# Optimization experiments

Hardware: AMD Instinct MI355X
Metric: run time of the kernel (lower is better)

## Reference

```python
import jax, jax.numpy as jnp
import numpy as np

QLEN, MLEN, CMLEN, BSZ, D_MODEL = 1024, 1024, 512, 2, 1024
N_HEAD, D_HEAD, D_INNER = 16, 64, 4096
KLEN = MLEN + CMLEN + QLEN
LN_EPS = 1e-5


def _layer_norm(x, scale, bias):
    mu = jnp.mean(x, axis=-1, keepdims=True)
    var = jnp.var(x, axis=-1, keepdims=True)
    return (x - mu) * jax.lax.rsqrt(var + LN_EPS) * scale + bias


def _rel_shift(x):
    # x: [qlen, klen, bsz, n_head]  (Transformer-XL relative shift)
    q, k, b, n = x.shape
    x = jnp.concatenate([jnp.zeros((q, 1, b, n), x.dtype), x], axis=1)
    x = x.reshape(k + 1, q, b, n)[1:]
    return x.reshape(q, k, b, n)


def setup_inputs() -> dict:
    key = jax.random.key(0)
    ks = jax.random.split(key, 10)
    s = 0.02
    # causal mask: query i (absolute pos MLEN_TOT+i) cannot attend to key j > MLEN_TOT+i
    mlen_tot = KLEN - QLEN
    i = jnp.arange(QLEN)[:, None]
    j = jnp.arange(KLEN)[None, :]
    attn_mask = j > (i + mlen_tot)
    return {
        "input_ids": jax.random.normal(ks[0], (QLEN, BSZ, D_MODEL), jnp.float32),
        "pos_emb": jax.random.normal(ks[1], (KLEN, D_MODEL), jnp.float32),
        "mem": jax.random.normal(ks[2], (MLEN, BSZ, D_MODEL), jnp.float32),
        "c_mem": jax.random.normal(ks[3], (CMLEN, BSZ, D_MODEL), jnp.float32),
        "attn_mask": attn_mask,
        "qkv_w": jax.random.normal(ks[4], (D_MODEL, 3 * N_HEAD * D_HEAD), jnp.float32) * s,
        "r_w": jax.random.normal(ks[5], (D_MODEL, N_HEAD * D_HEAD), jnp.float32) * s,
        "o_w": jax.random.normal(ks[6], (N_HEAD * D_HEAD, D_MODEL), jnp.float32) * s,
        "r_w_bias": jax.random.normal(ks[7], (N_HEAD, D_HEAD), jnp.float32) * s,
        "r_r_bias": jax.random.normal(ks[8], (N_HEAD, D_HEAD), jnp.float32) * s,
        "ln_attn_scale": jnp.ones((D_MODEL,), jnp.float32),
        "ln_attn_bias": jnp.zeros((D_MODEL,), jnp.float32),
        "ff_w1": jax.random.normal(ks[9], (D_MODEL, D_INNER), jnp.float32) * s,
        "ff_b1": jnp.zeros((D_INNER,), jnp.float32),
        "ff_w2": jax.random.normal(jax.random.fold_in(key, 11), (D_INNER, D_MODEL), jnp.float32) * s,
        "ff_b2": jnp.zeros((D_MODEL,), jnp.float32),
        "ln_ff_scale": jnp.ones((D_MODEL,), jnp.float32),
        "ln_ff_bias": jnp.zeros((D_MODEL,), jnp.float32),
    }


def reference(input_ids, pos_emb, mem, c_mem, attn_mask, qkv_w, r_w, o_w,
              r_w_bias, r_r_bias, ln_attn_scale, ln_attn_bias,
              ff_w1, ff_b1, ff_w2, ff_b2, ln_ff_scale, ln_ff_bias):
    qlen, bsz, d_model = input_ids.shape
    n_head, d_head = r_w_bias.shape
    scale = 1.0 / np.sqrt(d_head)

    # _concat_memories + cat with current sequence (seq-first, dim 0)
    mems = jnp.concatenate([mem, c_mem], axis=0)
    cat = jnp.concatenate([mems, input_ids], axis=0)          # [klen, b, d]

    w_heads = cat @ qkv_w                                     # [klen, b, 3*h*dh]
    w_q, w_k, w_v = jnp.split(w_heads, 3, axis=-1)
    w_q = w_q[-qlen:]
    klen = w_k.shape[0]

    w_q = w_q.reshape(qlen, bsz, n_head, d_head)
    w_k = w_k.reshape(klen, bsz, n_head, d_head)
    w_v = w_v.reshape(klen, bsz, n_head, d_head)
    r_k = (pos_emb @ r_w).reshape(klen, n_head, d_head)       # [klen, h, dh]

    AC = jnp.einsum('ibnd,jbnd->ijbn', w_q + r_w_bias, w_k)
    BD = jnp.einsum('ibnd,jnd->ijbn', w_q + r_r_bias, r_k)
    BD = _rel_shift(BD)
    attn_score = (AC + BD) * scale                            # [q, k, b, h]

    attn_score = jnp.where(attn_mask[:, :, None, None], jnp.float32(-1e30), attn_score)
    attn_prob = jax.nn.softmax(attn_score, axis=1)

    attn_vec = jnp.einsum('ijbn,jbnd->ibnd', attn_prob, w_v)
    attn_vec = attn_vec.reshape(qlen, bsz, n_head * d_head)
    attn_out = attn_vec @ o_w

    # post-lnorm residual (pre_lnorm=False)
    attn_res = _layer_norm(input_ids + attn_out, ln_attn_scale, ln_attn_bias)

    # PositionwiseFF (post-lnorm)
    h = jax.nn.relu(attn_res @ ff_w1 + ff_b1) @ ff_w2 + ff_b2
    out = _layer_norm(attn_res + h, ln_ff_scale, ln_ff_bias)
    return out
```

## Files before the change

kernel.cpp:

```cpp
#include <hip/hip_runtime.h>
#include <hip/hip_bf16.h>

#define QLEN 1024
#define KLEN 2560
#define MTOT 1536
#define BSZ 2
#define NH 16
#define DH 64
#define DMODEL 1024
#define DINNER 4096

typedef short bf16x8 __attribute__((ext_vector_type(8)));
typedef float f32x4  __attribute__((ext_vector_type(4)));

__device__ __forceinline__ short f2bf(float f) {
    union { float f; unsigned u; } v; v.f = f;
    unsigned r = v.u + 0x7FFFu + ((v.u >> 16) & 1u);
    return (short)(r >> 16);
}
__device__ __forceinline__ float bf2f(short s) {
    union { unsigned u; float f; } v; v.u = ((unsigned)(unsigned short)s) << 16;
    return v.f;
}
__device__ __forceinline__ unsigned pack2(float a, float b) {
    unsigned pk;
    asm("v_cvt_pk_bf16_f32 %0, %1, %2" : "=v"(pk) : "v"(a), "v"(b));
    return pk;
}

#define GLOAD16(g, l)                                                        \
    __builtin_amdgcn_global_load_lds(                                        \
        (const __attribute__((address_space(1))) unsigned int*)(g),          \
        (__attribute__((address_space(3))) unsigned int*)(l), 16, 0, 0)

__device__ __forceinline__ void tr_body(
    const float* __restrict__ in, short* __restrict__ out,
    int K, int N, int bx, int by, int tid, float (*ts)[65])
{
    const int k0 = by * 64, n0 = bx * 64;
    const int r = tid >> 2, cb = (tid & 3) * 16;
    #pragma unroll
    for (int u = 0; u < 16; u += 4) {
        const float4 v = *(const float4*)(in + (size_t)(k0 + r) * N + n0 + cb + u);
        ts[r][cb + u] = v.x; ts[r][cb + u + 1] = v.y;
        ts[r][cb + u + 2] = v.z; ts[r][cb + u + 3] = v.w;
    }
    __syncthreads();
    #pragma unroll
    for (int p = 0; p < 4; p++) {
        const int wr_ = (tid >> 4) + p * 16;
        const int c   = (tid & 15) * 4;
        uint2 pk;
        pk.x = pack2(ts[c][wr_], ts[c + 1][wr_]);
        pk.y = pack2(ts[c + 2][wr_], ts[c + 3][wr_]);
        *(uint2*)(out + (size_t)(n0 + wr_) * K + k0 + c) = pk;
    }
}

__global__ __launch_bounds__(256) void prep_all(
    const float* __restrict__ mem, const float* __restrict__ cmem,
    const float* __restrict__ inp, short* __restrict__ catb,
    const float* __restrict__ pos, short* __restrict__ posb,
    const float* __restrict__ qkv_w, short* __restrict__ qkv_wt,
    const float* __restrict__ r_w, short* __restrict__ r_wt,
    const float* __restrict__ o_w, short* __restrict__ o_wt,
    const float* __restrict__ ff_w1, short* __restrict__ ff1t,
    const float* __restrict__ ff_w2, short* __restrict__ ff2t)
{
    __shared__ float ts[64][65];
    const int bid = blockIdx.x;
    const int tid = threadIdx.x;
    if (bid < 2560) {
        const int i = bid * 256 + tid;
        const int row = i >> 7, c = (i & 127) * 8;
        const float* src;
        if (row < 2048)      src = mem  + (size_t)row * 1024;
        else if (row < 3072) src = cmem + (size_t)(row - 2048) * 1024;
        else                 src = inp  + (size_t)(row - 3072) * 1024;
        const float4 a = *(const float4*)(src + c);
        const float4 b = *(const float4*)(src + c + 4);
        uint4 o;
        o.x = pack2(a.x, a.y); o.y = pack2(a.z, a.w);
        o.z = pack2(b.x, b.y); o.w = pack2(b.z, b.w);
        *(uint4*)(catb + (size_t)i * 8) = o;
    } else if (bid < 3840) {
        const int i = (bid - 2560) * 256 + tid;
        const float4 a = *(const float4*)(pos + (size_t)i * 8);
        const float4 b = *(const float4*)(pos + (size_t)i * 8 + 4);
        uint4 o;
        o.x = pack2(a.x, a.y); o.y = pack2(a.z, a.w);
        o.z = pack2(b.x, b.y); o.w = pack2(b.z, b.w);
        *(uint4*)(posb + (size_t)i * 8) = o;
    } else if (bid < 4608) {
        const int r = bid - 3840; tr_body(qkv_w, qkv_wt, 1024, 3072, r % 48, r / 48, tid, ts);
    } else if (bid < 4864) {
        const int r = bid - 4608; tr_body(r_w, r_wt, 1024, 1024, r % 16, r / 16, tid, ts);
    } else if (bid < 5120) {
        const int r = bid - 4864; tr_body(o_w, o_wt, 1024, 1024, r % 16, r / 16, tid, ts);
    } else if (bid < 6144) {
        const int r = bid - 5120; tr_body(ff_w1, ff1t, 1024, 4096, r % 64, r / 64, tid, ts);
    } else {
        const int r = bid - 6144; tr_body(ff_w2, ff2t, 4096, 1024, r % 16, r / 16, tid, ts);
    }
}

__global__ __launch_bounds__(256) void vt_conv(
    const short* __restrict__ wh, short* __restrict__ vt)
{
    __shared__ short Ts[64][72];
    const int j0 = blockIdx.x * 64;
    const int bn = blockIdx.y;
    const int b = bn >> 4, n = bn & 15;
    const int tid = threadIdx.x;
    {
        const int key = tid >> 2, c = (tid & 3) * 16;
        const short* p = wh + ((size_t)(j0 + key) * BSZ + b) * 3072 + 2048 + n * 64 + c;
        *(bf16x8*)&Ts[key][c]     = *(const bf16x8*)p;
        *(bf16x8*)&Ts[key][c + 8] = *(const bf16x8*)(p + 8);
    }
    __syncthreads();
    {
        const int d = tid >> 2, kc = (tid & 3) * 16;
        __attribute__((aligned(16))) short tmp[16];
        #pragma unroll
        for (int u = 0; u < 16; u++) tmp[u] = Ts[kc + u][d];
        short* q = vt + ((size_t)(bn * 64) + d) * KLEN + j0 + kc;
        *(uint4*)q       = *(uint4*)tmp;
        *(uint4*)(q + 8) = *((uint4*)tmp + 1);
    }
}

__device__ __forceinline__ void gemm_core(
    const short* __restrict__ A, const short* __restrict__ Bt,
    short* As, short* Bs, int Kfull, int klen, int bm, int bn,
    int tid, f32x4 acc[4][4])
{
    const int w  = tid >> 6;
    const int l  = tid & 63;
    const int lg = l >> 4, lc = l & 15;
    const int wr = w >> 1, wc = w & 1;
    const int srow = 2 * w * 16 + (l >> 2);
    const int scol = (l & 3) * 8;
    const size_t aoff0 = (size_t)(bm + srow) * Kfull + scol;
    const size_t boff0 = (size_t)(bn + srow) * Kfull + scol;
    const size_t rstep = (size_t)16 * Kfull;
    short* lA0 = As + 2 * w * 512;
    short* lA1 = As + (2 * w + 1) * 512;
    short* lB0 = Bs + 2 * w * 512;
    short* lB1 = Bs + (2 * w + 1) * 512;

    for (int k0 = 0; k0 < klen; k0 += 32) {
        GLOAD16(A + aoff0 + k0, lA0);
        GLOAD16(A + aoff0 + rstep + k0, lA1);
        GLOAD16(Bt + boff0 + k0, lB0);
        GLOAD16(Bt + boff0 + rstep + k0, lB1);
        __syncthreads();
        bf16x8 af[4], bfr[4];
        #pragma unroll
        for (int m = 0; m < 4; m++)
            af[m] = *(const bf16x8*)(As + (wr * 64 + m * 16 + lc) * 32 + lg * 8);
        #pragma unroll
        for (int n = 0; n < 4; n++)
            bfr[n] = *(const bf16x8*)(Bs + (wc * 64 + n * 16 + lc) * 32 + lg * 8);
        #pragma unroll
        for (int m = 0; m < 4; m++)
            #pragma unroll
            for (int n = 0; n < 4; n++)
                acc[m][n] = __builtin_amdgcn_mfma_f32_16x16x32_bf16(
                    af[m], bfr[n], acc[m][n], 0, 0, 0);
        __syncthreads();
    }
}

__global__ __launch_bounds__(256) void gemm_g12(
    const short* __restrict__ catb, const short* __restrict__ qkv_wt,
    short* __restrict__ whb,
    const short* __restrict__ posb, const short* __restrict__ r_wt,
    short* __restrict__ rkb)
{
    __shared__ short As[4096], Bs[4096];
    const int tid = threadIdx.x;
    const int id0 = blockIdx.x;
    int id = (id0 & 7) * 116 + (id0 >> 3);
    const short *A, *Bt; short* Cb; int N, bm, bn;
    if (id < 384) {
        A = catb; Bt = qkv_wt; Cb = whb; N = 3072;
        bm = (id >> 4) * 128; bn = (8 + (id & 15)) * 128;
    } else if (id < 768) {
        id -= 384;
        A = catb; Bt = qkv_wt; Cb = whb; N = 3072;
        bm = (24 + id / 24) * 128; bn = (id % 24) * 128;
    } else {
        id -= 768;
        A = posb; Bt = r_wt; Cb = rkb; N = 1024;
        bm = (id / 8) * 128; bn = (id % 8) * 128;
    }

    f32x4 acc[4][4];
    #pragma unroll
    for (int m = 0; m < 4; m++)
        #pragma unroll
        for (int n = 0; n < 4; n++) acc[m][n] = (f32x4){0.f, 0.f, 0.f, 0.f};
    gemm_core(A, Bt, As, Bs, 1024, 1024, bm, bn, tid, acc);

    const int w = tid >> 6, l = tid & 63, lg = l >> 4, lc = l & 15;
    const int wr = w >> 1, wc = w & 1;
    #pragma unroll
    for (int m = 0; m < 4; m++)
        #pragma unroll
        for (int n = 0; n < 4; n++) {
            const int col = bn + wc * 64 + n * 16 + lc;
            #pragma unroll
            for (int r = 0; r < 4; r++) {
                const int row = bm + wr * 64 + m * 16 + lg * 4 + r;
                Cb[(size_t)row * N + col] = f2bf(acc[m][n][r]);
            }
        }
}

__global__ __launch_bounds__(256) void gemm_relu(
    const short* __restrict__ A, const short* __restrict__ Bt,
    const float* __restrict__ bias, short* __restrict__ Cb,
    int N, int K)
{
    __shared__ short As[4096], Bs[4096];
    const int tid = threadIdx.x;
    const int nbx = N >> 7;
    const int lid = blockIdx.x;
    const int nwg8 = gridDim.x >> 3;
    const int swz = (lid & 7) * nwg8 + (lid >> 3);
    const int bn = (swz % nbx) * 128, bm = (swz / nbx) * 128;
    f32x4 acc[4][4];
    #pragma unroll
    for (int m = 0; m < 4; m++)
        #pragma unroll
        for (int n = 0; n < 4; n++) acc[m][n] = (f32x4){0.f, 0.f, 0.f, 0.f};
    gemm_core(A, Bt, As, Bs, K, K, bm, bn, tid, acc);

    const int w = tid >> 6, l = tid & 63, lg = l >> 4, lc = l & 15;
    const int wr = w >> 1, wc = w & 1;
    #pragma unroll
    for (int m = 0; m < 4; m++)
        #pragma unroll
        for (int n = 0; n < 4; n++) {
            const int col = bn + wc * 64 + n * 16 + lc;
            const float bv = bias[col];
            #pragma unroll
            for (int r = 0; r < 4; r++) {
                const int row = bm + wr * 64 + m * 16 + lg * 4 + r;
                Cb[(size_t)row * N + col] = f2bf(fmaxf(acc[m][n][r] + bv, 0.0f));
            }
        }
}

__global__ __launch_bounds__(256) void gemm_split(
    const short* __restrict__ A, const short* __restrict__ Bt,
    float* __restrict__ C0, float* __restrict__ C1,
    int N, int Kfull, int Ksub)
{
    __shared__ short As[4096], Bs[4096];
    const int tid = threadIdx.x;
    const int nbx = N >> 7;
    const int lid = blockIdx.x;
    const int nwg8 = gridDim.x >> 3;
    const int swz = (lid & 7) * nwg8 + (lid >> 3);
    const int bn = (swz % nbx) * 128;
    const int rest = swz / nbx;
    const int bm = (rest & 15) * 128;
    const int z = rest >> 4;
    float* C = z ? C1 : C0;
    f32x4 acc[4][4];
    #pragma unroll
    for (int m = 0; m < 4; m++)
        #pragma unroll
        for (int n = 0; n < 4; n++) acc[m][n] = (f32x4){0.f, 0.f, 0.f, 0.f};
    gemm_core(A + z * Ksub, Bt + z * Ksub, As, Bs, Kfull, Ksub, bm, bn, tid, acc);

    const int w = tid >> 6, l = tid & 63, lg = l >> 4, lc = l & 15;
    const int wr = w >> 1, wc = w & 1;
    #pragma unroll
    for (int m = 0; m < 4; m++)
        #pragma unroll
        for (int n = 0; n < 4; n++) {
            const int col = bn + wc * 64 + n * 16 + lc;
            #pragma unroll
            for (int r = 0; r < 4; r++) {
                const int row = bm + wr * 64 + m * 16 + lg * 4 + r;
                C[(size_t)row * N + col] = acc[m][n][r];
            }
        }
}

__global__ __launch_bounds__(512, 2) void attn_mfma(
    const short* __restrict__ wh,
    const short* __restrict__ vt,
    const short* __restrict__ rk,
    const float* __restrict__ rwb,
    const float* __restrict__ rrb,
    short* __restrict__ po,
    float* __restrict__ ml)
{
    __shared__ __align__(16) short Ks[2][64 * 64];
    __shared__ __align__(16) short Vs[2][64 * 64];
    __shared__ __align__(16) short Rs[256 * 64];
    __shared__ __align__(16) short Ps[8][16 * 64];

    const int bid = blockIdx.x;
    const int ibp = (bid >> 3) & 7;
    const int z   = (bid >> 6) & 1;
    const int bn  = ((bid & 7) << 2) | (bid >> 7);
    const int i0  = ibp * 128;
    const int b   = bn >> 4, n = bn & 15;
    const int tid = threadIdx.x;
    const int w   = tid >> 6;
    const int l   = tid & 63;
    const int lg  = l >> 4;
    const int lc  = l & 15;
    const int i_base = i0 + 16 * w;

    bf16x8 aqw[2], aqr[2];
    {
        const int i = i_base + lc;
        const short* qp = wh + ((size_t)(MTOT + i) * BSZ + b) * 3072 + n * 64;
        #pragma unroll
        for (int kc2 = 0; kc2 < 2; kc2++) {
            const bf16x8 q8 = *(const bf16x8*)(qp + kc2 * 32 + lg * 8);
            const int d0 = kc2 * 32 + lg * 8;
            #pragma unroll
            for (int e = 0; e < 8; e++) {
                const float qv = bf2f(q8[e]);
                aqw[kc2][e] = f2bf(qv + rwb[n * 64 + d0 + e]);
                aqr[kc2][e] = f2bf(qv + rrb[n * 64 + d0 + e]);
            }
        }
    }

    f32x4 o_acc[4];
    #pragma unroll
    for (int nt = 0; nt < 4; nt++) o_acc[nt] = (f32x4){0.f, 0.f, 0.f, 0.f};
    float mrun[4]  = {0.f, 0.f, 0.f, 0.f};
    float lpart[4] = {0.f, 0.f, 0.f, 0.f};

    const int jend   = i0 + 1664;
    const int jhalf  = i0 / 2 + 832;
    const int jstart = z ? jhalf : 0;
    const int jstop  = z ? jend  : jhalf;

    const int kr = tid >> 3, kc = tid & 7;
    const size_t whK = (size_t)b * 3072 + 1024 + n * 64;
    const size_t vtK = (size_t)(bn * 64) * KLEN;
    const int mbase0 = jstart - i0 + 896;

    #pragma unroll
    for (int u = 0; u < 3; u++) {
        const int m = mbase0 + kr + 64 * u;
        bf16x8 rv = (bf16x8){0, 0, 0, 0, 0, 0, 0, 0};
        if (m < KLEN)
            rv = *(const bf16x8*)(rk + (size_t)m * 1024 + n * 64 + kc * 8);
        const int slot = m & 255;
        *(bf16x8*)(Rs + slot * 64 + ((kc ^ (slot & 7)) * 8)) = rv;
    }
    {
        const bf16x8 k0 = *(const bf16x8*)(wh + (size_t)(jstart + kr) * (BSZ * 3072) + whK + kc * 8);
        const bf16x8 v0 = *(const bf16x8*)(vt + vtK + (size_t)kr * KLEN + jstart + kc * 8);
        *(bf16x8*)(Ks[0] + kr * 64 + ((kc ^ (kr & 7)) * 8)) = k0;
        *(bf16x8*)(Vs[0] + kr * 64 + ((kc ^ (kr & 7)) * 8)) = v0;
    }
    bf16x8 pk = (bf16x8){0,0,0,0,0,0,0,0}, pv = pk, pr;
    {
        const int jn = jstart + 64;
        if (jn < jstop) {
            pk = *(const bf16x8*)(wh + (size_t)(jn + kr) * (BSZ * 3072) + whK + kc * 8);
            pv = *(const bf16x8*)(vt + vtK + (size_t)kr * KLEN + jn + kc * 8);
        }
        const int m = mbase0 + 192 + kr;
        pr = (m < KLEN) ? *(const bf16x8*)(rk + (size_t)m * 1024 + n * 64 + kc * 8)
                        : (bf16x8){0, 0, 0, 0, 0, 0, 0, 0};
    }

    int cur = 0;
    for (int j0 = jstart; j0 < jstop; j0 += 64) {
        const int mbase = j0 - i0 + 896;
        __syncthreads();
        *(bf16x8*)(Ks[cur ^ 1] + kr * 64 + ((kc ^ (kr & 7)) * 8)) = pk;
        *(bf16x8*)(Vs[cur ^ 1] + kr * 64 + ((kc ^ (kr & 7)) * 8)) = pv;
        {
            const int mw = mbase + 192 + kr;
            const int slot = mw & 255;
            *(bf16x8*)(Rs + slot * 64 + ((kc ^ (slot & 7)) * 8)) = pr;
        }
        {
            const int jn = j0 + 128;
            if (jn < jstop) {
                pk = *(const bf16x8*)(wh + (size_t)(jn + kr) * (BSZ * 3072) + whK + kc * 8);
                pv = *(const bf16x8*)(vt + vtK + (size_t)kr * KLEN + jn + kc * 8);
            }
            const int m = mbase + 256 + kr;
            pr = (m < KLEN) ? *(const bf16x8*)(rk + (size_t)m * 1024 + n * 64 + kc * 8)
                            : (bf16x8){0, 0, 0, 0, 0, 0, 0, 0};
        }

        __builtin_amdgcn_s_setprio(1);
        f32x4 sfr[4];
        #pragma unroll
        for (int jt = 0; jt < 4; jt++) {
            const int row = 16 * jt + lc;
            const int c0 = (lg ^ (row & 7)) * 8, c1 = ((4 + lg) ^ (row & 7)) * 8;
            const bf16x8 bk0 = *(const bf16x8*)(Ks[cur] + row * 64 + c0);
            const bf16x8 bk1 = *(const bf16x8*)(Ks[cur] + row * 64 + c1);
            f32x4 acc = (f32x4){0.f, 0.f, 0.f, 0.f};
            acc = __builtin_amdgcn_mfma_f32_16x16x32_bf16(aqw[0], bk0, acc, 0, 0, 0);
            acc = __builtin_amdgcn_mfma_f32_16x16x32_bf16(aqw[1], bk1, acc, 0, 0, 0);
            sfr[jt] = acc;
        }
        f32x4 dr[5];
        #pragma unroll
        for (int mt = 0; mt < 5; mt++) {
            const int slot = (mbase + 16 * mt + lc + 112 - 16 * w) & 255;
            const int c0 = (lg ^ (slot & 7)) * 8, c1 = ((4 + lg) ^ (slot & 7)) * 8;
            const bf16x8 br0 = *(const bf16x8*)(Rs + slot * 64 + c0);
            const bf16x8 br1 = *(const bf16x8*)(Rs + slot * 64 + c1);
            f32x4 acc = (f32x4){0.f, 0.f, 0.f, 0.f};
            acc = __builtin_amdgcn_mfma_f32_16x16x32_bf16(aqr[0], br0, acc, 0, 0, 0);
            acc = __builtin_amdgcn_mfma_f32_16x16x32_bf16(aqr[1], br1, acc, 0, 0, 0);
            dr[mt] = acc;
        }
        __builtin_amdgcn_s_setprio(0);

        #pragma unroll
        for (int r = 0; r < 4; r++) {
            const int q   = 4 * lg + r;
            const int o   = lc + 15 - q;
            const int src = (l & 48) | (o & 15);
            float sv[4];
            float mx = -1e30f;
            #pragma unroll
            for (int jt = 0; jt < 4; jt++) {
                const float v0 = __shfl(dr[jt][r], src);
                const float v1 = __shfl(dr[jt + 1][r], src);
                const float bd = (o < 16) ? v0 : v1;
                float s = (sfr[jt][r] + bd) * 0.125f;
                if (z) {
                    const int j = j0 + 16 * jt + lc;
                    if (j > i_base + q + MTOT) s = -1e30f;
                }
                sv[jt] = s;
                mx = fmaxf(mx, s);
            }
            if (__any(mx - mrun[r] > 8.0f)) {
                #pragma unroll
                for (int msk = 1; msk <= 8; msk <<= 1)
                    mx = fmaxf(mx, __shfl_xor(mx, msk));
                const float mnew = fmaxf(mrun[r], mx);
                const float corr = __expf(mrun[r] - mnew);
                mrun[r] = mnew;
                lpart[r] *= corr;
                #pragma unroll
                for (int nt = 0; nt < 4; nt++) o_acc[nt][r] *= corr;
            }
            float p0 = __expf(sv[0] - mrun[r]);
            float p1 = __expf(sv[1] - mrun[r]);
            float p2 = __expf(sv[2] - mrun[r]);
            float p3 = __expf(sv[3] - mrun[r]);
            lpart[r] += (p0 + p1) + (p2 + p3);
            const unsigned pk01 = pack2(p0, p1);
            const unsigned pk23 = pack2(p2, p3);
            short* pw = Ps[w] + q * 64 + (lc & 7);
            const int qs = q & 7;
            pw[(((0 + (lc >> 3)) ^ qs) * 8)] = (short)(pk01 & 0xffffu);
            pw[(((2 + (lc >> 3)) ^ qs) * 8)] = (short)(pk01 >> 16);
            pw[(((4 + (lc >> 3)) ^ qs) * 8)] = (short)(pk23 & 0xffffu);
            pw[(((6 + (lc >> 3)) ^ qs) * 8)] = (short)(pk23 >> 16);
        }

        asm volatile("s_waitcnt lgkmcnt(0)" ::: "memory");
        __builtin_amdgcn_sched_barrier(0);

        __builtin_amdgcn_s_setprio(1);
        const int pc0 = (lg ^ (lc & 7)) * 8, pc1 = ((4 + lg) ^ (lc & 7)) * 8;
        const bf16x8 pa0 = *(const bf16x8*)(Ps[w] + lc * 64 + pc0);
        const bf16x8 pa1 = *(const bf16x8*)(Ps[w] + lc * 64 + pc1);
        #pragma unroll
        for (int nt = 0; nt < 4; nt++) {
            const int row = 16 * nt + lc;
            const int c0 = (lg ^ (row & 7)) * 8, c1 = ((4 + lg) ^ (row & 7)) * 8;
            const bf16x8 bv0 = *(const bf16x8*)(Vs[cur] + row * 64 + c0);
            const bf16x8 bv1 = *(const bf16x8*)(Vs[cur] + row * 64 + c1);
            o_acc[nt] = __builtin_amdgcn_mfma_f32_16x16x32_bf16(pa0, bv0, o_acc[nt], 0, 0, 0);
            o_acc[nt] = __builtin_amdgcn_mfma_f32_16x16x32_bf16(pa1, bv1, o_acc[nt], 0, 0, 0);
        }
        __builtin_amdgcn_s_setprio(0);
        cur ^= 1;
    }

    const size_t blk = (size_t)z * 256 + ibp * 32 + bn;
    #pragma unroll
    for (int r = 0; r < 4; r++) {
        float lr = lpart[r];
        #pragma unroll
        for (int msk = 1; msk <= 8; msk <<= 1)
            lr += __shfl_xor(lr, msk);
        const int q = 16 * w + 4 * lg + r;
        #pragma unroll
        for (int nt = 0; nt < 4; nt++)
            po[(blk * 128 + q) * 64 + 16 * nt + lc] = f2bf(o_acc[nt][r]);
        if (lc == 0) {
            ml[(blk * 128 + q) * 2 + 0] = mrun[r];
            ml[(blk * 128 + q) * 2 + 1] = lr;
        }
    }
}

__global__ __launch_bounds__(256) void attn_merge(
    const short* __restrict__ po, const float* __restrict__ ml,
    short* __restrict__ av)
{
    const int blk = blockIdx.x;
    const int ib2 = blk >> 5, bn = blk & 31;
    const int b = bn >> 4, n = bn & 15;
    const int tid = threadIdx.x;
    const int q64 = tid >> 2, dc = (tid & 3) * 16;
    const int i = ib2 * 64 + q64;
    const size_t r0 = ((size_t)(i >> 7) * 32 + bn) * 128 + (i & 127);
    const size_t r1 = ((size_t)(256 + (i >> 7) * 32 + bn)) * 128 + (i & 127);
    const float m0 = ml[r0 * 2], l0 = ml[r0 * 2 + 1];
    const float m1 = ml[r1 * 2], l1 = ml[r1 * 2 + 1];
    const float M = fmaxf(m0, m1);
    const float c0 = __expf(m0 - M), c1 = __expf(m1 - M);
    const float invL = 1.0f / (l0 * c0 + l1 * c1);
    const bf16x8 a0 = *(const bf16x8*)(po + r0 * 64 + dc);
    const bf16x8 a1 = *(const bf16x8*)(po + r0 * 64 + dc + 8);
    const bf16x8 b0 = *(const bf16x8*)(po + r1 * 64 + dc);
    const bf16x8 b1 = *(const bf16x8*)(po + r1 * 64 + dc + 8);
    __attribute__((aligned(16))) short ov[16];
    #pragma unroll
    for (int e = 0; e < 8; e++) {
        ov[e]     = f2bf((bf2f(a0[e]) * c0 + bf2f(b0[e]) * c1) * invL);
        ov[e + 8] = f2bf((bf2f(a1[e]) * c0 + bf2f(b1[e]) * c1) * invL);
    }
    short* op = av + ((size_t)i * BSZ + b) * 1024 + n * 64 + dc;
    *(uint4*)op       = *(uint4*)ov;
    *(uint4*)(op + 8) = *((uint4*)ov + 1);
}

template <bool WB, bool HASB>
__global__ __launch_bounds__(256) void ln_fuse(
    const float* __restrict__ p0, const float* __restrict__ p1,
    const float* __restrict__ badd, const float* __restrict__ res,
    const float* __restrict__ scale, const float* __restrict__ bias,
    float* __restrict__ out, short* __restrict__ outb)
{
    const int row = blockIdx.x;
    const int tid = threadIdx.x;
    const size_t base = (size_t)row * 1024 + tid * 4;
    const float4 a = *(const float4*)(p0 + base);
    const float4 b = *(const float4*)(p1 + base);
    const float4 rv = *(const float4*)(res + base);
    float v[4] = {a.x + b.x + rv.x, a.y + b.y + rv.y,
                  a.z + b.z + rv.z, a.w + b.w + rv.w};
    if (HASB) {
        const float4 bb = *(const float4*)(badd + tid * 4);
        v[0] += bb.x; v[1] += bb.y; v[2] += bb.z; v[3] += bb.w;
    }
    float s  = v[0] + v[1] + v[2] + v[3];
    float ss = v[0]*v[0] + v[1]*v[1] + v[2]*v[2] + v[3]*v[3];
    #pragma unroll
    for (int off = 32; off >= 1; off >>= 1) {
        s  += __shfl_down(s, off);
        ss += __shfl_down(ss, off);
    }
    __shared__ float red[8];
    const int lane = tid & 63, wid = tid >> 6;
    if (lane == 0) { red[wid] = s; red[4 + wid] = ss; }
    __syncthreads();
    if (tid == 0) {
        red[0] = red[0] + red[1] + red[2] + red[3];
        red[4] = red[4] + red[5] + red[6] + red[7];
    }
    __syncthreads();
    const float mean = red[0] * (1.0f / 1024.0f);
    const float var  = red[4] * (1.0f / 1024.0f) - mean * mean;
    const float rstd = rsqrtf(var + 1e-5f);
    const float4 sc = *(const float4*)(scale + tid * 4);
    const float4 bi = *(const float4*)(bias + tid * 4);
    float4 o;
    o.x = (v[0] - mean) * rstd * sc.x + bi.x;
    o.y = (v[1] - mean) * rstd * sc.y + bi.y;
    o.z = (v[2] - mean) * rstd * sc.z + bi.z;
    o.w = (v[3] - mean) * rstd * sc.w + bi.w;
    *(float4*)(out + base) = o;
    if (WB) {
        uint2 pk;
        pk.x = pack2(o.x, o.y);
        pk.y = pack2(o.z, o.w);
        *(uint2*)(outb + base) = pk;
    }
}

extern "C" void kernel_launch(void* const* d_in, const int* in_sizes, int n_in,
                              void* d_out, int out_size, void* d_ws, size_t ws_size,
                              hipStream_t stream) {
    const float* input_ids = (const float*)d_in[0];
    const float* pos_emb   = (const float*)d_in[1];
    const float* mem       = (const float*)d_in[2];
    const float* c_mem     = (const float*)d_in[3];
    const float* qkv_w     = (const float*)d_in[5];
    const float* r_w       = (const float*)d_in[6];
    const float* o_w       = (const float*)d_in[7];
    const float* r_w_bias  = (const float*)d_in[8];
    const float* r_r_bias  = (const float*)d_in[9];
    const float* ln_a_s    = (const float*)d_in[10];
    const float* ln_a_b    = (const float*)d_in[11];
    const float* ff_w1     = (const float*)d_in[12];
    const float* ff_b1     = (const float*)d_in[13];
    const float* ff_w2     = (const float*)d_in[14];
    const float* ff_b2     = (const float*)d_in[15];
    const float* ln_f_s    = (const float*)d_in[16];
    const float* ln_f_b    = (const float*)d_in[17];

    char* base = (char*)d_ws;
    short* o_wt   = (short*)(base + 0);
    short* ff1t   = (short*)(base + 2097152);
    short* ff2t   = (short*)(base + 10485760);
    short* whb    = (short*)(base + 18874368);
    short* rkb    = (short*)(base + 50331648);
    short* qkv_wt = (short*)(base + 55574528);
    short* catb   = (short*)(base + 61865984);
    short* posb   = (short*)(base + 72351744);
    short* r_wt   = (short*)(base + 77594624);
    short* vtb    = (short*)(base + 55574528);
    short* po     = (short*)(base + 66060288);
    float* mlb    = (float*)(base + 74448896);
    short* avb    = (short*)(base + 74973184);
    float* hp0    = (float*)(base + 18874368);
    float* hp1    = (float*)(base + 27262976);
    float* ares   = (float*)(base + 35651584);
    short* aresb  = (short*)(base + 44040192);
    short* h1b    = (short*)(base + 48234496);

    const dim3 thr(256);

    prep_all<<<dim3(7168), thr, 0, stream>>>(
        mem, c_mem, input_ids, catb, pos_emb, posb,
        qkv_w, qkv_wt, r_w, r_wt, o_w, o_wt, ff_w1, ff1t, ff_w2, ff2t);
    gemm_g12<<<dim3(928), thr, 0, stream>>>(catb, qkv_wt, whb, posb, r_wt, rkb);
    vt_conv<<<dim3(40, 32), thr, 0, stream>>>(whb, vtb);
    attn_mfma<<<dim3(512), dim3(512), 0, stream>>>(
        whb, vtb, rkb, r_w_bias, r_r_bias, po, mlb);
    attn_merge<<<dim3(512), thr, 0, stream>>>(po, mlb, avb);
    gemm_split<<<dim3(256), thr, 0, stream>>>(
        avb, o_wt, hp0, hp1, 1024, 1024, 512);
    ln_fuse<true, false><<<dim3(2048), thr, 0, stream>>>(
        hp0, hp1, nullptr, input_ids, ln_a_s, ln_a_b, ares, aresb);
    gemm_relu<<<dim3(512), thr, 0, stream>>>(aresb, ff1t, ff_b1, h1b, 4096, 1024);
    gemm_split<<<dim3(256), thr, 0, stream>>>(
        h1b, ff2t, hp0, hp1, 1024, 4096, 2048);
    ln_fuse<false, true><<<dim3(2048), thr, 0, stream>>>(
        hp0, hp1, ff_b2, ares, ln_f_s, ln_f_b, (float*)d_out, nullptr);
}
```

Before: 273.9 us.

## Double-buffer GEMM LDS tiles and fold softmax scale into log2-domain query

The shared GEMM core now double-buffers its LDS tiles. It prefetches the next K-slice while computing the current one, which drops one barrier per iteration and doubles LDS per block. The attention kernel pre-scales the biased queries by scale*log2(e) and switches all softmax exponentials, including those in the merge kernel, to native exp2. It also hoists the five rel-shift shuffles out of the inner loop. These changes target global-load latency in the GEMMs and ALU work in attention, at the cost of LDS occupancy and a slight bf16 rounding change from pre-scaling q.

```diff
diff --git a/kernel.cpp b/kernel.cpp
--- a/kernel.cpp
+++ b/kernel.cpp
@@ -9,6 +9,8 @@
 #define DH 64
 #define DMODEL 1024
 #define DINNER 4096
+
+#define SCL2E 0.18033688011112042f
 
 typedef short bf16x8 __attribute__((ext_vector_type(8)));
 typedef float f32x4  __attribute__((ext_vector_type(4)));
@@ -144,24 +146,31 @@
     const size_t aoff0 = (size_t)(bm + srow) * Kfull + scol;
     const size_t boff0 = (size_t)(bn + srow) * Kfull + scol;
     const size_t rstep = (size_t)16 * Kfull;
-    short* lA0 = As + 2 * w * 512;
-    short* lA1 = As + (2 * w + 1) * 512;
-    short* lB0 = Bs + 2 * w * 512;
-    short* lB1 = Bs + (2 * w + 1) * 512;
-
+    const int ch0 = 2 * w * 512, ch1 = (2 * w + 1) * 512;
+
+    GLOAD16(A + aoff0, As + ch0);
+    GLOAD16(A + aoff0 + rstep, As + ch1);
+    GLOAD16(Bt + boff0, Bs + ch0);
+    GLOAD16(Bt + boff0 + rstep, Bs + ch1);
+    __syncthreads();
+
+    int cur = 0;
     for (int k0 = 0; k0 < klen; k0 += 32) {
-        GLOAD16(A + aoff0 + k0, lA0);
-        GLOAD16(A + aoff0 + rstep + k0, lA1);
-        GLOAD16(Bt + boff0 + k0, lB0);
-        GLOAD16(Bt + boff0 + rstep + k0, lB1);
-        __syncthreads();
+        const int nb = (cur ^ 1) * 4096;
+        if (k0 + 32 < klen) {
+            GLOAD16(A + aoff0 + k0 + 32, As + nb + ch0);
+            GLOAD16(A + aoff0 + rstep + k0 + 32, As + nb + ch1);
+            GLOAD16(Bt + boff0 + k0 + 32, Bs + nb + ch0);
+            GLOAD16(Bt + boff0 + rstep + k0 + 32, Bs + nb + ch1);
+        }
+        const int cb = cur * 4096;
         bf16x8 af[4], bfr[4];
         #pragma unroll
         for (int m = 0; m < 4; m++)
-            af[m] = *(const bf16x8*)(As + (wr * 64 + m * 16 + lc) * 32 + lg * 8);
+            af[m] = *(const bf16x8*)(As + cb + (wr * 64 + m * 16 + lc) * 32 + lg * 8);
         #pragma unroll
         for (int n = 0; n < 4; n++)
-            bfr[n] = *(const bf16x8*)(Bs + (wc * 64 + n * 16 + lc) * 32 + lg * 8);
+            bfr[n] = *(const bf16x8*)(Bs + cb + (wc * 64 + n * 16 + lc) * 32 + lg * 8);
         #pragma unroll
         for (int m = 0; m < 4; m++)
             #pragma unroll
@@ -169,6 +178,7 @@
                 acc[m][n] = __builtin_amdgcn_mfma_f32_16x16x32_bf16(
                     af[m], bfr[n], acc[m][n], 0, 0, 0);
         __syncthreads();
+        cur ^= 1;
     }
 }
 
@@ -178,7 +188,7 @@
     const short* __restrict__ posb, const short* __restrict__ r_wt,
     short* __restrict__ rkb)
 {
-    __shared__ short As[4096], Bs[4096];
+    __shared__ short As[8192], Bs[8192];
     const int tid = threadIdx.x;
     const int id0 = blockIdx.x;
     int id = (id0 & 7) * 116 + (id0 >> 3);
@@ -223,7 +233,7 @@
     const float* __restrict__ bias, short* __restrict__ Cb,
     int N, int K)
 {
-    __shared__ short As[4096], Bs[4096];
+    __shared__ short As[8192], Bs[8192];
     const int tid = threadIdx.x;
     const int nbx = N >> 7;
     const int lid = blockIdx.x;
@@ -258,7 +268,7 @@
     float* __restrict__ C0, float* __restrict__ C1,
     int N, int Kfull, int Ksub)
 {
-    __shared__ short As[4096], Bs[4096];
+    __shared__ short As[8192], Bs[8192];
     const int tid = threadIdx.x;
     const int nbx = N >> 7;
     const int lid = blockIdx.x;
@@ -329,8 +339,8 @@
             #pragma unroll
             for (int e = 0; e < 8; e++) {
                 const float qv = bf2f(q8[e]);
-                aqw[kc2][e] = f2bf(qv + rwb[n * 64 + d0 + e]);
-                aqr[kc2][e] = f2bf(qv + rrb[n * 64 + d0 + e]);
+                aqw[kc2][e] = f2bf((qv + rwb[n * 64 + d0 + e]) * SCL2E);
+                aqr[kc2][e] = f2bf((qv + rrb[n * 64 + d0 + e]) * SCL2E);
             }
         }
     }
@@ -432,14 +442,15 @@
             const int q   = 4 * lg + r;
             const int o   = lc + 15 - q;
             const int src = (l & 48) | (o & 15);
+            float sh[5];
+            #pragma unroll
+            for (int t = 0; t < 5; t++) sh[t] = __shfl(dr[t][r], src);
             float sv[4];
             float mx = -1e30f;
             #pragma unroll
             for (int jt = 0; jt < 4; jt++) {
-                const float v0 = __shfl(dr[jt][r], src);
-                const float v1 = __shfl(dr[jt + 1][r], src);
-                const float bd = (o < 16) ? v0 : v1;
-                float s = (sfr[jt][r] + bd) * 0.125f;
+                const float bd = (o < 16) ? sh[jt] : sh[jt + 1];
+                float s = sfr[jt][r] + bd;
                 if (z) {
                     const int j = j0 + 16 * jt + lc;
                     if (j > i_base + q + MTOT) s = -1e30f;
@@ -452,16 +463,16 @@
                 for (int msk = 1; msk <= 8; msk <<= 1)
                     mx = fmaxf(mx, __shfl_xor(mx, msk));
                 const float mnew = fmaxf(mrun[r], mx);
-                const float corr = __expf(mrun[r] - mnew);
+                const float corr = __builtin_amdgcn_exp2f(mrun[r] - mnew);
                 mrun[r] = mnew;
                 lpart[r] *= corr;
                 #pragma unroll
                 for (int nt = 0; nt < 4; nt++) o_acc[nt][r] *= corr;
             }
-            float p0 = __expf(sv[0] - mrun[r]);
-            float p1 = __expf(sv[1] - mrun[r]);
-            float p2 = __expf(sv[2] - mrun[r]);
-            float p3 = __expf(sv[3] - mrun[r]);
+            const float p0 = __builtin_amdgcn_exp2f(sv[0] - mrun[r]);
+            const float p1 = __builtin_amdgcn_exp2f(sv[1] - mrun[r]);
+            const float p2 = __builtin_amdgcn_exp2f(sv[2] - mrun[r]);
+            const float p3 = __builtin_amdgcn_exp2f(sv[3] - mrun[r]);
             lpart[r] += (p0 + p1) + (p2 + p3);
             const unsigned pk01 = pack2(p0, p1);
             const unsigned pk23 = pack2(p2, p3);
@@ -526,7 +537,8 @@
     const float m0 = ml[r0 * 2], l0 = ml[r0 * 2 + 1];
     const float m1 = ml[r1 * 2], l1 = ml[r1 * 2 + 1];
     const float M = fmaxf(m0, m1);
-    const float c0 = __expf(m0 - M), c1 = __expf(m1 - M);
+    const float c0 = __builtin_amdgcn_exp2f(m0 - M);
+    const float c1 = __builtin_amdgcn_exp2f(m1 - M);
     const float invL = 1.0f / (l0 * c0 + l1 * c1);
     const bf16x8 a0 = *(const bf16x8*)(po + r0 * 64 + dc);
     const bf16x8 a1 = *(const bf16x8*)(po + r0 * 64 + dc + 8);
```

Result: slower. 289.0 us (+5.5%).
